# Kernel optimization log

Measured on AMD Instinct MI355X. Metric: run time of the kernel, lower is better.

Reference implementation:

```python
import jax, jax.numpy as jnp
import numpy as np
import math

N_HEADS = 8
LN_EPS = 1e-5

def _layernorm(x, g, b):
    m = jnp.mean(x, axis=-1, keepdims=True)
    v = jnp.var(x, axis=-1, keepdims=True)
    return (x - m) / jnp.sqrt(v + LN_EPS) * g + b

def _elu_feature(x):
    return jax.nn.elu(x) + 1.0

def _recurrence(Q, K, V, decay, reverse):
    # Q,K,V: (B,H,T,d); decay: (H,)
    B, H, T, d = Q.shape
    lamS = decay[None, :, None, None]
    lamz = decay[None, :, None]
    def step(carry, inp):
        S, z = carry
        q, k, v = inp
        S = lamS * S + k[..., :, None] * v[..., None, :]       # (B,H,d,d)
        z = lamz * z + k                                        # (B,H,d)
        y_raw = jnp.einsum('bhd,bhde->bhe', q, S)
        c_raw = jnp.sum(q * z, axis=-1)
        qk = jnp.sum(q * k, axis=-1, keepdims=True)
        return (S, z), (y_raw - 0.5 * qk * v, c_raw - 0.5 * qk[..., 0])
    S0 = jnp.zeros((B, H, d, d), Q.dtype)
    z0 = jnp.zeros((B, H, d), Q.dtype)
    qs = jnp.moveaxis(Q, 2, 0)
    ks = jnp.moveaxis(K, 2, 0)
    vs = jnp.moveaxis(V, 2, 0)
    _, (Y, C) = jax.lax.scan(step, (S0, z0), (qs, ks, vs), reverse=reverse)
    return jnp.moveaxis(Y, 0, 2), jnp.moveaxis(C, 0, 2)  # (B,H,T,d),(B,H,T)

def setup_inputs() -> dict:
    B, T, D, F = 2, 2048, 512, 2048
    key = jax.random.key(0)
    ks = jax.random.split(key, 8)
    std = 0.02
    return {
        'x': jax.random.normal(ks[0], (B, T, D), jnp.float32),
        'mask': jnp.zeros((B, T), dtype=bool),
        'Wq': jax.random.normal(ks[1], (D, D), jnp.float32) * std,
        'Wk': jax.random.normal(ks[2], (D, D), jnp.float32) * std,
        'Wv': jax.random.normal(ks[3], (D, D), jnp.float32) * std,
        'Wo': jax.random.normal(ks[4], (D, D), jnp.float32) * std,
        'bo': jnp.zeros((D,), jnp.float32),
        'g1': jnp.ones((D,), jnp.float32),
        'b1': jnp.zeros((D,), jnp.float32),
        'g2': jnp.ones((D,), jnp.float32),
        'b2': jnp.zeros((D,), jnp.float32),
        'W1': jax.random.normal(ks[5], (F, D), jnp.float32) * std,
        'bf1': jnp.zeros((F,), jnp.float32),
        'W2': jax.random.normal(ks[6], (D, F), jnp.float32) * std,
        'bf2': jnp.zeros((D,), jnp.float32),
        'decay_logit': jnp.full((N_HEADS,), math.log(9.0), jnp.float32),
    }

def reference(x, mask, Wq, Wk, Wv, Wo, bo, g1, b1, g2, b2, W1, bf1, W2, bf2, decay_logit):
    B, T, D = x.shape
    H = N_HEADS
    hd = D // H
    residual = x
    xn = _layernorm(x, g1, b1)
    def proj(W):
        return jnp.einsum('btd,od->bto', xn, W).reshape(B, T, H, hd).transpose(0, 2, 1, 3)
    Q = _elu_feature(proj(Wq))
    K = _elu_feature(proj(Wk))
    V = proj(Wv)
    pad = (~mask).astype(x.dtype)[:, None, :, None]  # (B,1,T,1)
    K = K * pad
    V = V * pad
    decay = jax.nn.sigmoid(decay_logit)
    Yf, Cf = _recurrence(Q, K, V, decay, reverse=False)
    Yb, Cb = _recurrence(Q, K, V, decay, reverse=True)
    denom = jnp.clip((Cf + Cb)[..., None], 1e-6)
    out = (Yf + Yb) / denom                       # (B,H,T,d)
    out = out.transpose(0, 2, 1, 3).reshape(B, T, D)
    out = jnp.einsum('btd,od->bto', out, Wo) + bo
    x = residual + out
    h = _layernorm(x, g2, b2)
    ffn = jnp.einsum('btd,fd->btf', h, W1) + bf1
    ffn = jax.nn.gelu(ffn, approximate=False)
    ffn = jnp.einsum('btf,df->btd', ffn, W2) + bf2
    return x + ffn
```

## Files before the change

kernel.cpp:

```cpp
#include <hip/hip_runtime.h>
#include <math.h>

#define BB 2
#define TT 2048
#define DD 512
#define FF 2048
#define HH 8
#define BT 4096
#define NC 32
#define CK 64

typedef __bf16 bf16_t;
typedef bf16_t bf16x8 __attribute__((ext_vector_type(8)));
typedef bf16_t bf16x4 __attribute__((ext_vector_type(4)));
typedef float f32x4 __attribute__((ext_vector_type(4)));

typedef const __attribute__((address_space(1))) void* gas_p;
typedef __attribute__((address_space(3))) void* las_p;

__device__ __forceinline__ void async16(const void* g, void* l) {
  __builtin_amdgcn_global_load_lds((gas_p)g, (las_p)l, 16, 0, 0);
}

#define PIPE_SYNC(vm) asm volatile("s_waitcnt lgkmcnt(0) vmcnt(" vm ")\n\ts_barrier" ::: "memory")

__global__ __launch_bounds__(256) void ln_cast_kernel(
    const float* __restrict__ x, const float* __restrict__ g, const float* __restrict__ bb,
    bf16_t* __restrict__ out,
    const float* __restrict__ Wq, const float* __restrict__ Wk,
    const float* __restrict__ Wv, const float* __restrict__ Wo,
    const float* __restrict__ W1, const float* __restrict__ W2,
    bf16_t* __restrict__ wdst) {
  int t = threadIdx.x;
  if (blockIdx.x >= 1024) {
    size_t i = ((size_t)(blockIdx.x - 1024) * 256 + t) * 8;
    const float* src; size_t off;
    if (i < 262144)       { src = Wq; off = i; }
    else if (i < 524288)  { src = Wk; off = i - 262144; }
    else if (i < 786432)  { src = Wv; off = i - 524288; }
    else if (i < 1048576) { src = Wo; off = i - 786432; }
    else if (i < 2097152) { src = W1; off = i - 1048576; }
    else                  { src = W2; off = i - 2097152; }
    float4 a = *(const float4*)(src + off);
    float4 b = *(const float4*)(src + off + 4);
    bf16x8 o;
    o[0] = (bf16_t)a.x; o[1] = (bf16_t)a.y; o[2] = (bf16_t)a.z; o[3] = (bf16_t)a.w;
    o[4] = (bf16_t)b.x; o[5] = (bf16_t)b.y; o[6] = (bf16_t)b.z; o[7] = (bf16_t)b.w;
    *(bf16x8*)(wdst + i) = o;
    return;
  }
  int w = t >> 6, l = t & 63;
  int row = blockIdx.x * 4 + w;
  int c0 = l * 8;
  const float* xr = x + (size_t)row * DD + c0;
  float4 a = *(const float4*)xr;
  float4 b4 = *(const float4*)(xr + 4);
  float s  = a.x + a.y + a.z + a.w + b4.x + b4.y + b4.z + b4.w;
  float sq = a.x*a.x + a.y*a.y + a.z*a.z + a.w*a.w +
             b4.x*b4.x + b4.y*b4.y + b4.z*b4.z + b4.w*b4.w;
  for (int o = 32; o; o >>= 1) { s += __shfl_xor(s, o); sq += __shfl_xor(sq, o); }
  float m = s * (1.f / 512.f);
  float var = sq * (1.f / 512.f) - m * m;
  float r = rsqrtf(var + 1e-5f);
  float4 ga = *(const float4*)(g + c0);  float4 gb = *(const float4*)(g + c0 + 4);
  float4 ba = *(const float4*)(bb + c0); float4 bbv = *(const float4*)(bb + c0 + 4);
  bf16x8 o8;
  o8[0] = (bf16_t)((a.x - m) * r * ga.x + ba.x);
  o8[1] = (bf16_t)((a.y - m) * r * ga.y + ba.y);
  o8[2] = (bf16_t)((a.z - m) * r * ga.z + ba.z);
  o8[3] = (bf16_t)((a.w - m) * r * ga.w + ba.w);
  o8[4] = (bf16_t)((b4.x - m) * r * gb.x + bbv.x);
  o8[5] = (bf16_t)((b4.y - m) * r * gb.y + bbv.y);
  o8[6] = (bf16_t)((b4.z - m) * r * gb.z + bbv.z);
  o8[7] = (bf16_t)((b4.w - m) * r * gb.w + bbv.w);
  *(bf16x8*)(out + (size_t)row * DD + c0) = o8;
}

__global__ __launch_bounds__(256) void ln2_kernel(
    const float* __restrict__ x2, const float* __restrict__ g, const float* __restrict__ bb,
    bf16_t* __restrict__ out) {
  int t = threadIdx.x;
  int w = t >> 6, l = t & 63;
  int row = blockIdx.x * 4 + w;
  int c0 = l * 8;
  const float* xr = x2 + (size_t)row * DD + c0;
  float4 a = *(const float4*)xr;
  float4 b4 = *(const float4*)(xr + 4);
  float s  = a.x + a.y + a.z + a.w + b4.x + b4.y + b4.z + b4.w;
  float sq = a.x*a.x + a.y*a.y + a.z*a.z + a.w*a.w +
             b4.x*b4.x + b4.y*b4.y + b4.z*b4.z + b4.w*b4.w;
  for (int o = 32; o; o >>= 1) { s += __shfl_xor(s, o); sq += __shfl_xor(sq, o); }
  float m = s * (1.f / 512.f);
  float var = sq * (1.f / 512.f) - m * m;
  float r = rsqrtf(var + 1e-5f);
  float4 ga = *(const float4*)(g + c0);  float4 gb = *(const float4*)(g + c0 + 4);
  float4 ba = *(const float4*)(bb + c0); float4 bbv = *(const float4*)(bb + c0 + 4);
  bf16x8 o8;
  o8[0] = (bf16_t)((a.x - m) * r * ga.x + ba.x);
  o8[1] = (bf16_t)((a.y - m) * r * ga.y + ba.y);
  o8[2] = (bf16_t)((a.z - m) * r * ga.z + ba.z);
  o8[3] = (bf16_t)((a.w - m) * r * ga.w + ba.w);
  o8[4] = (bf16_t)((b4.x - m) * r * gb.x + bbv.x);
  o8[5] = (bf16_t)((b4.y - m) * r * gb.y + bbv.y);
  o8[6] = (bf16_t)((b4.z - m) * r * gb.z + bbv.z);
  o8[7] = (bf16_t)((b4.w - m) * r * gb.w + bbv.w);
  *(bf16x8*)(out + (size_t)row * DD + c0) = o8;
}

template<int MODE>
__global__ __launch_bounds__(256) void mfma_gemm(
    const bf16_t* __restrict__ A, const bf16_t* __restrict__ B, int K, int NT,
    bf16_t* __restrict__ Qo, bf16_t* __restrict__ Ko, bf16_t* __restrict__ Vo,
    bf16_t* __restrict__ Ob, const float* __restrict__ bias,
    const unsigned char* __restrict__ mask) {
  __shared__ __align__(16) bf16_t smem[3 * 8192];
  int tid = threadIdx.x;
  int bid = blockIdx.x;
  int xcd = bid & 7;
  int tmp = bid >> 3;
  int nt = tmp % NT;
  int mt = (tmp / NT) * 8 + xcd;
  int n0 = nt * 128, m0 = mt * 128;
  int elt = tid * 8;
  int srow = elt >> 5, scol = elt & 31;
  const bf16_t* Ag = A + (size_t)(m0 + srow) * K + scol;
  const bf16_t* Bg = B + (size_t)(n0 + srow) * K + scol;
  size_t hstep = (size_t)64 * K;
  int NS = K >> 5;
#define ISSUE(s) { bf16_t* st = smem + ((s) % 3) * 8192; int k0 = (s) * 32; \
    async16(Ag + k0, st + elt); async16(Ag + k0 + hstep, st + 2048 + elt); \
    async16(Bg + k0, st + 4096 + elt); async16(Bg + k0 + hstep, st + 6144 + elt); }
  ISSUE(0); ISSUE(1);
  f32x4 acc[4][4] = {};
  int w = tid >> 6, l = tid & 63;
  int wm = (w >> 1) * 64, wn = (w & 1) * 64;
  int fr = l & 15, fk = (l >> 4) * 8;
  for (int i = 0; i < NS; i++) {
    if (i < NS - 1) PIPE_SYNC("4");
    else            PIPE_SYNC("0");
    if (i + 2 < NS) ISSUE(i + 2);
    const bf16_t* As = smem + (i % 3) * 8192;
    const bf16_t* Bs = As + 4096;
    bf16x8 af[4], bfr[4];
#pragma unroll
    for (int ii = 0; ii < 4; ii++) af[ii] = *(const bf16x8*)&As[(wm + ii * 16 + fr) * 32 + fk];
#pragma unroll
    for (int j = 0; j < 4; j++) bfr[j] = *(const bf16x8*)&Bs[(wn + j * 16 + fr) * 32 + fk];
#pragma unroll
    for (int ii = 0; ii < 4; ii++)
#pragma unroll
      for (int j = 0; j < 4; j++)
        acc[ii][j] = __builtin_amdgcn_mfma_f32_16x16x32_bf16(af[ii], bfr[j], acc[ii][j], 0, 0, 0);
  }
#undef ISSUE
  __syncthreads();
  const int CST = 136;
  int cn = l & 15, cr = (l >> 4) * 4;
  bf16_t* outp;
  int ldc, ncol0;
  if (MODE == 0) {
    int seg = n0 >> 9;
    outp = seg == 0 ? Qo : (seg == 1 ? Ko : Vo);
    ldc = 512; ncol0 = n0 & 511;
  } else {
    outp = Ob; ldc = 2048; ncol0 = n0;
  }
#pragma unroll
  for (int i = 0; i < 4; i++) {
#pragma unroll
    for (int r = 0; r < 4; r++) {
      int mrow = wm + i * 16 + cr + r;
      float p = 1.f;
      if (MODE == 0) p = mask[m0 + mrow] ? 0.f : 1.f;
#pragma unroll
      for (int j = 0; j < 4; j++) {
        int ncol = wn + j * 16 + cn;
        float v = acc[i][j][r];
        float ov;
        if (MODE == 0) {
          int seg = n0 >> 9;
          float e = v > 0.f ? v + 1.f : expf(v);
          ov = seg == 0 ? e : (seg == 1 ? e * p : v * p);
        } else {
          float t2 = v + bias[ncol0 + ncol];
          ov = 0.5f * t2 * (1.f + erff(t2 * 0.70710678118654752f));
        }
        smem[mrow * CST + ncol] = (bf16_t)ov;
      }
    }
  }
  __syncthreads();
#pragma unroll
  for (int it = 0; it < 8; it++) {
    int vec = tid + it * 256;
    int row = vec >> 4;
    int col = (vec & 15) * 8;
    bf16x8 v8 = *(const bf16x8*)&smem[row * CST + col];
    *(bf16x8*)(outp + (size_t)(m0 + row) * ldc + ncol0 + col) = v8;
  }
}

template<int MODE>
__global__ __launch_bounds__(256) void gemm64(
    const bf16_t* __restrict__ A, const bf16_t* __restrict__ B, int K, int NT,
    bf16_t* __restrict__ Qo, bf16_t* __restrict__ Ko, bf16_t* __restrict__ Vo,
    const float* __restrict__ bias, const float* __restrict__ resid,
    float* __restrict__ fout, const unsigned char* __restrict__ mask) {
  __shared__ __align__(16) bf16_t smem[4 * 6144];
  int tid = threadIdx.x;
  int bid = blockIdx.x;
  int xcd = bid & 7;
  int tmp = bid >> 3;
  int nt = tmp % NT;
  int mt = (tmp / NT) * 8 + xcd;
  int n0 = nt * 64, m0 = mt * 128;
  int elt = tid * 8;
  int srow = elt >> 5, scol = elt & 31;
  const bf16_t* Ag = A + (size_t)(m0 + srow) * K + scol;
  const bf16_t* Bg = B + (size_t)(n0 + srow) * K + scol;
  size_t hstep = (size_t)64 * K;
  const int NS = K >> 5;
#define ISSUE(s) { bf16_t* st = smem + ((s) & 3) * 6144; int k0 = (s) * 32; \
    async16(Ag + k0, st + elt); async16(Ag + k0 + hstep, st + 2048 + elt); \
    async16(Bg + k0, st + 4096 + elt); }
  ISSUE(0); ISSUE(1); ISSUE(2);
  f32x4 acc[4][2] = {};
  int w = tid >> 6, l = tid & 63;
  int wm = (w >> 1) * 64, wn = (w & 1) * 32;
  int fr = l & 15, fk = (l >> 4) * 8;
  for (int i = 0; i < NS; i++) {
    int rem = NS - 1 - i;
    if (rem >= 2)      PIPE_SYNC("6");
    else if (rem == 1) PIPE_SYNC("3");
    else               PIPE_SYNC("0");
    if (i + 3 < NS) ISSUE(i + 3);
    const bf16_t* As = smem + (i & 3) * 6144;
    const bf16_t* Bs = As + 4096;
    bf16x8 af[4], bfr[2];
#pragma unroll
    for (int ii = 0; ii < 4; ii++) af[ii] = *(const bf16x8*)&As[(wm + ii * 16 + fr) * 32 + fk];
#pragma unroll
    for (int j = 0; j < 2; j++) bfr[j] = *(const bf16x8*)&Bs[(wn + j * 16 + fr) * 32 + fk];
#pragma unroll
    for (int ii = 0; ii < 4; ii++)
#pragma unroll
      for (int j = 0; j < 2; j++)
        acc[ii][j] = __builtin_amdgcn_mfma_f32_16x16x32_bf16(af[ii], bfr[j], acc[ii][j], 0, 0, 0);
  }
#undef ISSUE
  __syncthreads();
  int cn = l & 15, cr = (l >> 4) * 4;
  if (MODE == 0) {
    const int CST = 72;
    int seg = n0 >> 9;
#pragma unroll
    for (int i = 0; i < 4; i++) {
#pragma unroll
      for (int r = 0; r < 4; r++) {
        int mrow = wm + i * 16 + cr + r;
        float p = mask[m0 + mrow] ? 0.f : 1.f;
#pragma unroll
        for (int j = 0; j < 2; j++) {
          int ncol = wn + j * 16 + cn;
          float v = acc[i][j][r];
          float e = v > 0.f ? v + 1.f : expf(v);
          float ov = seg == 0 ? e : (seg == 1 ? e * p : v * p);
          smem[mrow * CST + ncol] = (bf16_t)ov;
        }
      }
    }
    __syncthreads();
    bf16_t* outp = seg == 0 ? Qo : (seg == 1 ? Ko : Vo);
    int ncol0 = n0 & 511;
#pragma unroll
    for (int it = 0; it < 4; it++) {
      int vec = tid + it * 256;
      int row = vec >> 3;
      int col = (vec & 7) * 8;
      bf16x8 v8 = *(const bf16x8*)&smem[row * CST + col];
      *(bf16x8*)(outp + (size_t)(m0 + row) * 512 + ncol0 + col) = v8;
    }
  } else {
    const int FST = 72;
    float* smf = (float*)smem;
#pragma unroll
    for (int i = 0; i < 4; i++)
#pragma unroll
      for (int r = 0; r < 4; r++) {
        int mrow = wm + i * 16 + cr + r;
#pragma unroll
        for (int j = 0; j < 2; j++) {
          int ncol = wn + j * 16 + cn;
          smf[mrow * FST + ncol] = acc[i][j][r];
        }
      }
    __syncthreads();
#pragma unroll
    for (int it = 0; it < 8; it++) {
      int vec = tid + it * 256;
      int row = vec >> 4;
      int col = (vec & 15) * 4;
      size_t gidx = (size_t)(m0 + row) * 512 + n0 + col;
      float4 v = *(const float4*)&smf[row * FST + col];
      float4 bi = *(const float4*)(bias + n0 + col);
      float4 rr = *(const float4*)(resid + gidx);
      *(float4*)(fout + gidx) = make_float4(v.x + bi.x + rr.x, v.y + bi.y + rr.y,
                                            v.z + bi.z + rr.z, v.w + bi.w + rr.w);
    }
  }
}

__global__ __launch_bounds__(256) void chunk_summary_kernel(
    const bf16_t* __restrict__ Kb, const bf16_t* __restrict__ Vb,
    const float* __restrict__ dl, bf16_t* __restrict__ Sst, float* __restrict__ zst) {
  int chunk = blockIdx.x, bh = blockIdx.y;
  int b = bh >> 3, h = bh & 7;
  int t0 = chunk * CK;
  int tid = threadIdx.x;
  const int ST = 72;
  __shared__ __align__(16) bf16_t KTf[64 * ST];
  __shared__ __align__(16) bf16_t KTb[64 * ST];
  __shared__ __align__(16) bf16_t VT [64 * ST];
  float lam = 1.f / (1.f + expf(-dl[h]));
  int lrow = tid >> 2, lq = tid & 3;
  float wf = powf(lam, (float)(63 - lrow));
  float wb = powf(lam, (float)lrow);
#pragma unroll
  for (int q = 0; q < 2; q++) {
    int c = lq * 16 + q * 8;
    size_t gidx = ((size_t)(b * TT + t0 + lrow)) * DD + (size_t)h * 64 + c;
    bf16x8 k8 = *(const bf16x8*)(Kb + gidx);
    bf16x8 v8 = *(const bf16x8*)(Vb + gidx);
#pragma unroll
    for (int u = 0; u < 8; u++) {
      float kv = (float)k8[u];
      KTf[(c + u) * ST + lrow] = (bf16_t)(kv * wf);
      KTb[(c + u) * ST + lrow] = (bf16_t)(kv * wb);
      VT [(c + u) * ST + lrow] = v8[u];
    }
  }
  __syncthreads();
  int w = tid >> 6, l = tid & 63;
  int dir = w >> 1;
  int drow = (w & 1) * 32;
  const bf16_t* KT = dir ? KTb : KTf;
  int fr = l & 15, fk = (l >> 4) * 8;
  bf16x8 afrag[2][2], bfrag[4][2];
#pragma unroll
  for (int ti = 0; ti < 2; ti++) {
    afrag[ti][0] = *(const bf16x8*)&KT[(drow + ti * 16 + fr) * ST + fk];
    afrag[ti][1] = *(const bf16x8*)&KT[(drow + ti * 16 + fr) * ST + 32 + fk];
  }
#pragma unroll
  for (int tj = 0; tj < 4; tj++) {
    bfrag[tj][0] = *(const bf16x8*)&VT[(tj * 16 + fr) * ST + fk];
    bfrag[tj][1] = *(const bf16x8*)&VT[(tj * 16 + fr) * ST + 32 + fk];
  }
  f32x4 acc[2][4] = {};
#pragma unroll
  for (int ti = 0; ti < 2; ti++)
#pragma unroll
    for (int tj = 0; tj < 4; tj++) {
      acc[ti][tj] = __builtin_amdgcn_mfma_f32_16x16x32_bf16(afrag[ti][0], bfrag[tj][0], acc[ti][tj], 0, 0, 0);
      acc[ti][tj] = __builtin_amdgcn_mfma_f32_16x16x32_bf16(afrag[ti][1], bfrag[tj][1], acc[ti][tj], 0, 0, 0);
    }
  if (tid < 128) {
    const bf16_t* KTz = (tid >> 6) ? KTb : KTf;
    int d = tid & 63;
    float z = 0.f;
    for (int j = 0; j < 64; j += 8) {
      bf16x8 kz = *(const bf16x8*)&KTz[d * ST + j];
#pragma unroll
      for (int u = 0; u < 8; u++) z += (float)kz[u];
    }
    zst[(((size_t)(tid >> 6) * 16 + bh) * NC + chunk) * 64 + d] = z;
  }
  __syncthreads();
  bf16_t* Ss = dir ? KTb : KTf;
  int cr = (l >> 4) * 4, cn = l & 15;
#pragma unroll
  for (int ti = 0; ti < 2; ti++)
#pragma unroll
    for (int tj = 0; tj < 4; tj++)
#pragma unroll
      for (int r = 0; r < 4; r++) {
        int d = drow + ti * 16 + cr + r;
        int e = tj * 16 + cn;
        Ss[e * ST + d] = (bf16_t)acc[ti][tj][r];
      }
  __syncthreads();
  size_t bfr = ((size_t)bh * NC + chunk) * 4096;
  size_t bbr = (((size_t)16 + bh) * NC + chunk) * 4096;
#pragma unroll
  for (int it = 0; it < 4; it++) {
    int vec = tid + it * 256;
    int d2 = vec >> 9;
    int idx = vec & 511;
    int row = idx >> 3, col = (idx & 7) * 8;
    bf16x8 v8 = *(const bf16x8*)((d2 ? KTb : KTf) + row * ST + col);
    *(bf16x8*)(Sst + (d2 ? bbr : bfr) + (size_t)row * 64 + col) = v8;
  }
}

__global__ __launch_bounds__(256) void scan_kernel(bf16_t* __restrict__ Sst,
                                                   float* __restrict__ zst,
                                                   const float* __restrict__ dl) {
  int sub = blockIdx.x;
  int bh  = blockIdx.y;
  int dir = blockIdx.z;
  int h = bh & 7;
  int tid = threadIdx.x;
  float lam = 1.f / (1.f + expf(-dl[h]));
  float lamC = powf(lam, 64.f);
  int elem = sub * 256 + tid;
  size_t base = ((size_t)dir * 16 + bh) * (size_t)NC * 4096 + elem;
  float s = 0.f;
  for (int g = 0; g < 4; g++) {
    bf16_t L[8];
#pragma unroll
    for (int i = 0; i < 8; i++) {
      int st = g * 8 + i;
      int c = dir ? (NC - 1 - st) : st;
      L[i] = Sst[base + (size_t)c * 4096];
    }
#pragma unroll
    for (int i = 0; i < 8; i++) {
      int st = g * 8 + i;
      int c = dir ? (NC - 1 - st) : st;
      s = s * lamC + (float)L[i];
      Sst[base + (size_t)c * 4096] = (bf16_t)s;
    }
  }
  if (sub == 0 && tid < 64) {
    size_t zb = ((size_t)dir * 16 + bh) * (size_t)NC * 64 + tid;
    float z = 0.f;
    for (int g = 0; g < 4; g++) {
      float zL[8];
#pragma unroll
      for (int i = 0; i < 8; i++) {
        int st = g * 8 + i;
        int c = dir ? (NC - 1 - st) : st;
        zL[i] = zst[zb + (size_t)c * 64];
      }
#pragma unroll
      for (int i = 0; i < 8; i++) {
        int st = g * 8 + i;
        int c = dir ? (NC - 1 - st) : st;
        z = z * lamC + zL[i];
        zst[zb + (size_t)c * 64] = z;
      }
    }
  }
}

#define AST 72
__global__ __launch_bounds__(256) void chunk_attn_kernel(
    const bf16_t* __restrict__ Qb, const bf16_t* __restrict__ Kb, const bf16_t* __restrict__ Vb,
    const bf16_t* __restrict__ Sst, const float* __restrict__ zst, const float* __restrict__ dl,
    bf16_t* __restrict__ attnb) {
  int chunk = blockIdx.x, bh = blockIdx.y;
  int b = bh >> 3, h = bh & 7;
  int t0 = chunk * CK;
  int tid = threadIdx.x;
  __shared__ __align__(16) bf16_t Qa[64 * AST];
  __shared__ __align__(16) bf16_t KA[64 * AST];
  __shared__ __align__(16) bf16_t Vt[64 * AST];
  __shared__ __align__(16) bf16_t Sft[64 * AST];
  __shared__ __align__(16) bf16_t Sbt[64 * AST];
  __shared__ float rowpart[64][16];
  __shared__ float zpf[64], zpb[64];
  __shared__ float den[64];
  __shared__ float pw[72];
  float lam = 1.f / (1.f + expf(-dl[h]));
  if (tid <= 64) pw[tid] = powf(lam, (float)tid);
  int lrow = tid >> 2, lq = tid & 3;
  for (int q = 0; q < 2; q++) {
    int c = lq * 16 + q * 8;
    size_t g = ((size_t)(b * TT + t0 + lrow)) * DD + (size_t)h * 64 + c;
    bf16x8 q8 = *(const bf16x8*)(Qb + g);
    bf16x8 k8 = *(const bf16x8*)(Kb + g);
    bf16x8 v8 = *(const bf16x8*)(Vb + g);
    *(bf16x8*)&Qa[lrow * AST + c] = q8;
    *(bf16x8*)&KA[lrow * AST + c] = k8;
#pragma unroll
    for (int u = 0; u < 8; u++) Vt[(c + u) * AST + lrow] = v8[u];
  }
  {
    int c16 = lq * 16;
    if (chunk > 0) {
      const bf16_t* src = Sst + ((size_t)bh * NC + chunk - 1) * 4096 + (size_t)lrow * 64 + c16;
      *(bf16x8*)&Sft[lrow * AST + c16] = *(const bf16x8*)src;
      *(bf16x8*)&Sft[lrow * AST + c16 + 8] = *(const bf16x8*)(src + 8);
      if (tid < 64) zpf[tid] = zst[((size_t)bh * NC + chunk - 1) * 64 + tid];
    } else {
      bf16x8 z8 = {};
      *(bf16x8*)&Sft[lrow * AST + c16] = z8;
      *(bf16x8*)&Sft[lrow * AST + c16 + 8] = z8;
      if (tid < 64) zpf[tid] = 0.f;
    }
    if (chunk < NC - 1) {
      const bf16_t* src = Sst + (((size_t)16 + bh) * NC + chunk + 1) * 4096 + (size_t)lrow * 64 + c16;
      *(bf16x8*)&Sbt[lrow * AST + c16] = *(const bf16x8*)src;
      *(bf16x8*)&Sbt[lrow * AST + c16 + 8] = *(const bf16x8*)(src + 8);
      if (tid < 64) zpb[tid] = zst[(((size_t)16 + bh) * NC + chunk + 1) * 64 + tid];
    } else {
      bf16x8 z8 = {};
      *(bf16x8*)&Sbt[lrow * AST + c16] = z8;
      *(bf16x8*)&Sbt[lrow * AST + c16 + 8] = z8;
      if (tid < 64) zpb[tid] = 0.f;
    }
  }
  __syncthreads();
  int w = tid >> 6, l = tid & 63;
  int fr = l & 15, fk = (l >> 4) * 8;
  int cr = (l >> 4) * 4, cn = l & 15;
  int ms = w * 16;
  bf16x8 qf0 = *(const bf16x8*)&Qa[(ms + fr) * AST + fk];
  bf16x8 qf1 = *(const bf16x8*)&Qa[(ms + fr) * AST + 32 + fk];
  f32x4 aqk[4] = {};
#pragma unroll
  for (int t = 0; t < 4; t++) {
    bf16x8 kf0 = *(const bf16x8*)&KA[(t * 16 + fr) * AST + fk];
    bf16x8 kf1 = *(const bf16x8*)&KA[(t * 16 + fr) * AST + 32 + fk];
    aqk[t] = __builtin_amdgcn_mfma_f32_16x16x32_bf16(qf0, kf0, aqk[t], 0, 0, 0);
    aqk[t] = __builtin_amdgcn_mfma_f32_16x16x32_bf16(qf1, kf1, aqk[t], 0, 0, 0);
  }
  __syncthreads();
  float rs[4] = {0.f, 0.f, 0.f, 0.f};
#pragma unroll
  for (int t = 0; t < 4; t++) {
#pragma unroll
    for (int r = 0; r < 4; r++) {
      int i = ms + cr + r;
      int j = t * 16 + cn;
      int dd = i > j ? i - j : j - i;
      float v = aqk[t][r] * pw[dd];
      rs[r] += v;
      KA[i * AST + j] = (bf16_t)v;
    }
  }
#pragma unroll
  for (int r = 0; r < 4; r++) rowpart[ms + cr + r][cn] = rs[r];
  __syncthreads();
  bf16x8 af0 = *(const bf16x8*)&KA[(ms + fr) * AST + fk];
  bf16x8 af1 = *(const bf16x8*)&KA[(ms + fr) * AST + 32 + fk];
  f32x4 aY[4] = {}, aSf[4] = {}, aSb[4] = {};
#pragma unroll
  for (int t = 0; t < 4; t++) {
    bf16x8 vf0 = *(const bf16x8*)&Vt[(t * 16 + fr) * AST + fk];
    bf16x8 vf1 = *(const bf16x8*)&Vt[(t * 16 + fr) * AST + 32 + fk];
    aY[t] = __builtin_amdgcn_mfma_f32_16x16x32_bf16(af0, vf0, aY[t], 0, 0, 0);
    aY[t] = __builtin_amdgcn_mfma_f32_16x16x32_bf16(af1, vf1, aY[t], 0, 0, 0);
    bf16x8 sf0 = *(const bf16x8*)&Sft[(t * 16 + fr) * AST + fk];
    bf16x8 sf1 = *(const bf16x8*)&Sft[(t * 16 + fr) * AST + 32 + fk];
    aSf[t] = __builtin_amdgcn_mfma_f32_16x16x32_bf16(qf0, sf0, aSf[t], 0, 0, 0);
    aSf[t] = __builtin_amdgcn_mfma_f32_16x16x32_bf16(qf1, sf1, aSf[t], 0, 0, 0);
    bf16x8 sb0 = *(const bf16x8*)&Sbt[(t * 16 + fr) * AST + fk];
    bf16x8 sb1 = *(const bf16x8*)&Sbt[(t * 16 + fr) * AST + 32 + fk];
    aSb[t] = __builtin_amdgcn_mfma_f32_16x16x32_bf16(qf0, sb0, aSb[t], 0, 0, 0);
    aSb[t] = __builtin_amdgcn_mfma_f32_16x16x32_bf16(qf1, sb1, aSb[t], 0, 0, 0);
  }
  {
    int i = tid >> 2, p = tid & 3;
    float s = 0.f;
#pragma unroll
    for (int xx = 0; xx < 4; xx++) s += rowpart[i][p * 4 + xx];
    float czf = 0.f, czb = 0.f;
#pragma unroll
    for (int cc = 0; cc < 2; cc++) {
      int c = p * 16 + cc * 8;
      bf16x8 q8 = *(const bf16x8*)&Qa[i * AST + c];
#pragma unroll
      for (int u = 0; u < 8; u++) { czf += (float)q8[u] * zpf[c + u]; czb += (float)q8[u] * zpb[c + u]; }
    }
    float dsum = s + pw[i + 1] * czf + pw[64 - i] * czb;
    dsum += __shfl_xor(dsum, 1);
    dsum += __shfl_xor(dsum, 2);
    if (p == 0) den[i] = dsum;
  }
  __syncthreads();
#pragma unroll
  for (int t = 0; t < 4; t++) {
#pragma unroll
    for (int r = 0; r < 4; r++) {
      int i = ms + cr + r;
      int e = t * 16 + cn;
      float lrf = pw[i + 1], lrb = pw[64 - i];
      float inv = 1.f / fmaxf(den[i], 1e-6f);
      float val = (aY[t][r] + lrf * aSf[t][r] + lrb * aSb[t][r]) * inv;
      attnb[((size_t)(b * TT + t0 + i)) * DD + (size_t)h * 64 + e] = (bf16_t)val;
    }
  }
}

extern "C" void kernel_launch(void* const* d_in, const int* in_sizes, int n_in,
                              void* d_out, int out_size, void* d_ws, size_t ws_size,
                              hipStream_t stream) {
  const float* x   = (const float*)d_in[0];
  const unsigned char* mask = (const unsigned char*)d_in[1];
  const float* Wq  = (const float*)d_in[2];
  const float* Wk  = (const float*)d_in[3];
  const float* Wv  = (const float*)d_in[4];
  const float* Wo  = (const float*)d_in[5];
  const float* bo  = (const float*)d_in[6];
  const float* g1  = (const float*)d_in[7];
  const float* b1  = (const float*)d_in[8];
  const float* g2  = (const float*)d_in[9];
  const float* b2  = (const float*)d_in[10];
  const float* W1  = (const float*)d_in[11];
  const float* bf1 = (const float*)d_in[12];
  const float* W2  = (const float*)d_in[13];
  const float* bf2 = (const float*)d_in[14];
  const float* dl  = (const float*)d_in[15];
  float* out = (float*)d_out;

  float* ws = (float*)d_ws;
  const size_t U = (size_t)BT * DD;
  float* Qr  = ws;
  float* Kr  = ws + U;
  float* Vr  = ws + 2 * U;
  float* R3  = ws + 3 * U;
  float* R4  = ws + 4 * U;
  float* x2  = ws + 5 * U;
  bf16_t* Sstb = (bf16_t*)(ws + 6 * U);
  float* zst = ws + 8 * U;
  bf16_t* wall = (bf16_t*)(ws + 8 * U + 131072);
  bf16_t* Qb    = (bf16_t*)Qr;
  bf16_t* Kb    = (bf16_t*)Kr;
  bf16_t* Vb    = (bf16_t*)Vr;
  bf16_t* xnb   = (bf16_t*)R3;
  bf16_t* attnb = (bf16_t*)R4;
  bf16_t* h2b   = (bf16_t*)Qr;
  bf16_t* ffn1b = (bf16_t*)Kr;
  bf16_t* Wob = wall + 786432;
  bf16_t* W1b = wall + 1048576;
  bf16_t* W2b = wall + 2097152;

  ln_cast_kernel<<<1024 + 1536, 256, 0, stream>>>(x, g1, b1, xnb, Wq, Wk, Wv, Wo, W1, W2, wall);
  gemm64<0><<<768, 256, 0, stream>>>(xnb, wall, 512, 24, Qb, Kb, Vb,
                                     nullptr, nullptr, nullptr, mask);
  chunk_summary_kernel<<<dim3(NC, 16), 256, 0, stream>>>(Kb, Vb, dl, Sstb, zst);
  scan_kernel<<<dim3(16, 16, 2), 256, 0, stream>>>(Sstb, zst, dl);
  chunk_attn_kernel<<<dim3(NC, 16), 256, 0, stream>>>(Qb, Kb, Vb, Sstb, zst, dl, attnb);
  gemm64<1><<<256, 256, 0, stream>>>(attnb, Wob, 512, 8, nullptr, nullptr, nullptr,
                                     bo, x, x2, nullptr);
  ln2_kernel<<<1024, 256, 0, stream>>>(x2, g2, b2, h2b);
  mfma_gemm<2><<<512, 256, 0, stream>>>(h2b, W1b, 512, 16, nullptr, nullptr, nullptr,
                                        ffn1b, bf1, nullptr);
  gemm64<1><<<256, 256, 0, stream>>>(ffn1b, W2b, 2048, 8, nullptr, nullptr, nullptr,
                                     bf2, x2, out, nullptr);
}
```

Measured before the change: 184.3 us.

## Fuse chunk summary, scan and chunk attention into one cooperative kernel

Merges the three attention-stage kernels into one cooperative kernel of 512 blocks, using grid-wide syncs between the chunk-summary, inter-chunk scan and intra-chunk attention phases. Q, K and V are loaded into shared memory once and reused, instead of being reloaded by separate launches. This removes two kernel launch boundaries and the associated reloads, at the cost of grid-sync overhead, higher shared-memory use per block, and a requirement that all 512 blocks be co-resident.

```diff
diff --git a/kernel.cpp b/kernel.cpp
--- a/kernel.cpp
+++ b/kernel.cpp
@@ -1,4 +1,5 @@
 #include <hip/hip_runtime.h>
+#include <hip/hip_cooperative_groups.h>
 #include <math.h>
 
 #define BB 2
@@ -310,18 +311,27 @@
   }
 }
 
-__global__ __launch_bounds__(256) void chunk_summary_kernel(
-    const bf16_t* __restrict__ Kb, const bf16_t* __restrict__ Vb,
-    const float* __restrict__ dl, bf16_t* __restrict__ Sst, float* __restrict__ zst) {
-  int chunk = blockIdx.x, bh = blockIdx.y;
+#define MST 72
+__global__ __launch_bounds__(256, 2) void attn_mega_kernel(
+    const bf16_t* __restrict__ Qb, const bf16_t* __restrict__ Kb, const bf16_t* __restrict__ Vb,
+    const float* __restrict__ dl, bf16_t* __restrict__ Sst, float* __restrict__ zst,
+    bf16_t* __restrict__ attnb) {
+  __shared__ __align__(16) bf16_t KT2[2][64 * MST];
+  __shared__ __align__(16) bf16_t VT [64 * MST];
+  __shared__ __align__(16) bf16_t KA [64 * MST];
+  __shared__ __align__(16) bf16_t Qa [64 * MST];
+  __shared__ __align__(16) bf16_t Sft[64 * MST];
+  __shared__ __align__(16) bf16_t Sbt[64 * MST];
+  __shared__ float rowpart[64][16];
+  __shared__ float zpf[64], zpb[64], den[64];
+  __shared__ float pw[72];
+  int tid = threadIdx.x;
+  int bid = blockIdx.x;
+  int chunk = bid & 31, bh = bid >> 5;
   int b = bh >> 3, h = bh & 7;
   int t0 = chunk * CK;
-  int tid = threadIdx.x;
-  const int ST = 72;
-  __shared__ __align__(16) bf16_t KTf[64 * ST];
-  __shared__ __align__(16) bf16_t KTb[64 * ST];
-  __shared__ __align__(16) bf16_t VT [64 * ST];
   float lam = 1.f / (1.f + expf(-dl[h]));
+  if (tid <= 64) pw[tid] = powf(lam, (float)tid);
   int lrow = tid >> 2, lq = tid & 3;
   float wf = powf(lam, (float)(63 - lrow));
   float wb = powf(lam, (float)lrow);
@@ -329,199 +339,165 @@
   for (int q = 0; q < 2; q++) {
     int c = lq * 16 + q * 8;
     size_t gidx = ((size_t)(b * TT + t0 + lrow)) * DD + (size_t)h * 64 + c;
+    bf16x8 q8 = *(const bf16x8*)(Qb + gidx);
     bf16x8 k8 = *(const bf16x8*)(Kb + gidx);
     bf16x8 v8 = *(const bf16x8*)(Vb + gidx);
+    *(bf16x8*)&Qa[lrow * MST + c] = q8;
+    *(bf16x8*)&KA[lrow * MST + c] = k8;
 #pragma unroll
     for (int u = 0; u < 8; u++) {
       float kv = (float)k8[u];
-      KTf[(c + u) * ST + lrow] = (bf16_t)(kv * wf);
-      KTb[(c + u) * ST + lrow] = (bf16_t)(kv * wb);
-      VT [(c + u) * ST + lrow] = v8[u];
+      KT2[0][(c + u) * MST + lrow] = (bf16_t)(kv * wf);
+      KT2[1][(c + u) * MST + lrow] = (bf16_t)(kv * wb);
+      VT [(c + u) * MST + lrow] = v8[u];
     }
   }
   __syncthreads();
   int w = tid >> 6, l = tid & 63;
   int dir = w >> 1;
   int drow = (w & 1) * 32;
-  const bf16_t* KT = dir ? KTb : KTf;
   int fr = l & 15, fk = (l >> 4) * 8;
-  bf16x8 afrag[2][2], bfrag[4][2];
-#pragma unroll
-  for (int ti = 0; ti < 2; ti++) {
-    afrag[ti][0] = *(const bf16x8*)&KT[(drow + ti * 16 + fr) * ST + fk];
-    afrag[ti][1] = *(const bf16x8*)&KT[(drow + ti * 16 + fr) * ST + 32 + fk];
-  }
-#pragma unroll
-  for (int tj = 0; tj < 4; tj++) {
-    bfrag[tj][0] = *(const bf16x8*)&VT[(tj * 16 + fr) * ST + fk];
-    bfrag[tj][1] = *(const bf16x8*)&VT[(tj * 16 + fr) * ST + 32 + fk];
-  }
-  f32x4 acc[2][4] = {};
-#pragma unroll
-  for (int ti = 0; ti < 2; ti++)
+  int cr = (l >> 4) * 4, cn = l & 15;
+  {
+    const bf16_t* KT = KT2[dir];
+    bf16x8 afrag[2][2], bfrag[4][2];
+#pragma unroll
+    for (int ti = 0; ti < 2; ti++) {
+      afrag[ti][0] = *(const bf16x8*)&KT[(drow + ti * 16 + fr) * MST + fk];
+      afrag[ti][1] = *(const bf16x8*)&KT[(drow + ti * 16 + fr) * MST + 32 + fk];
+    }
 #pragma unroll
     for (int tj = 0; tj < 4; tj++) {
-      acc[ti][tj] = __builtin_amdgcn_mfma_f32_16x16x32_bf16(afrag[ti][0], bfrag[tj][0], acc[ti][tj], 0, 0, 0);
-      acc[ti][tj] = __builtin_amdgcn_mfma_f32_16x16x32_bf16(afrag[ti][1], bfrag[tj][1], acc[ti][tj], 0, 0, 0);
-    }
-  if (tid < 128) {
-    const bf16_t* KTz = (tid >> 6) ? KTb : KTf;
-    int d = tid & 63;
-    float z = 0.f;
-    for (int j = 0; j < 64; j += 8) {
-      bf16x8 kz = *(const bf16x8*)&KTz[d * ST + j];
-#pragma unroll
-      for (int u = 0; u < 8; u++) z += (float)kz[u];
-    }
-    zst[(((size_t)(tid >> 6) * 16 + bh) * NC + chunk) * 64 + d] = z;
-  }
-  __syncthreads();
-  bf16_t* Ss = dir ? KTb : KTf;
-  int cr = (l >> 4) * 4, cn = l & 15;
-#pragma unroll
-  for (int ti = 0; ti < 2; ti++)
-#pragma unroll
-    for (int tj = 0; tj < 4; tj++)
-#pragma unroll
-      for (int r = 0; r < 4; r++) {
-        int d = drow + ti * 16 + cr + r;
-        int e = tj * 16 + cn;
-        Ss[e * ST + d] = (bf16_t)acc[ti][tj][r];
-      }
-  __syncthreads();
-  size_t bfr = ((size_t)bh * NC + chunk) * 4096;
-  size_t bbr = (((size_t)16 + bh) * NC + chunk) * 4096;
-#pragma unroll
-  for (int it = 0; it < 4; it++) {
-    int vec = tid + it * 256;
-    int d2 = vec >> 9;
-    int idx = vec & 511;
-    int row = idx >> 3, col = (idx & 7) * 8;
-    bf16x8 v8 = *(const bf16x8*)((d2 ? KTb : KTf) + row * ST + col);
-    *(bf16x8*)(Sst + (d2 ? bbr : bfr) + (size_t)row * 64 + col) = v8;
-  }
-}
-
-__global__ __launch_bounds__(256) void scan_kernel(bf16_t* __restrict__ Sst,
-                                                   float* __restrict__ zst,
-                                                   const float* __restrict__ dl) {
-  int sub = blockIdx.x;
-  int bh  = blockIdx.y;
-  int dir = blockIdx.z;
-  int h = bh & 7;
-  int tid = threadIdx.x;
-  float lam = 1.f / (1.f + expf(-dl[h]));
-  float lamC = powf(lam, 64.f);
-  int elem = sub * 256 + tid;
-  size_t base = ((size_t)dir * 16 + bh) * (size_t)NC * 4096 + elem;
-  float s = 0.f;
-  for (int g = 0; g < 4; g++) {
-    bf16_t L[8];
-#pragma unroll
-    for (int i = 0; i < 8; i++) {
-      int st = g * 8 + i;
-      int c = dir ? (NC - 1 - st) : st;
-      L[i] = Sst[base + (size_t)c * 4096];
-    }
-#pragma unroll
-    for (int i = 0; i < 8; i++) {
-      int st = g * 8 + i;
-      int c = dir ? (NC - 1 - st) : st;
-      s = s * lamC + (float)L[i];
-      Sst[base + (size_t)c * 4096] = (bf16_t)s;
-    }
-  }
-  if (sub == 0 && tid < 64) {
-    size_t zb = ((size_t)dir * 16 + bh) * (size_t)NC * 64 + tid;
-    float z = 0.f;
+      bfrag[tj][0] = *(const bf16x8*)&VT[(tj * 16 + fr) * MST + fk];
+      bfrag[tj][1] = *(const bf16x8*)&VT[(tj * 16 + fr) * MST + 32 + fk];
+    }
+    f32x4 acc[2][4] = {};
+#pragma unroll
+    for (int ti = 0; ti < 2; ti++)
+#pragma unroll
+      for (int tj = 0; tj < 4; tj++) {
+        acc[ti][tj] = __builtin_amdgcn_mfma_f32_16x16x32_bf16(afrag[ti][0], bfrag[tj][0], acc[ti][tj], 0, 0, 0);
+        acc[ti][tj] = __builtin_amdgcn_mfma_f32_16x16x32_bf16(afrag[ti][1], bfrag[tj][1], acc[ti][tj], 0, 0, 0);
+      }
+    if (tid < 128) {
+      const bf16_t* KTz = KT2[tid >> 6];
+      int d = tid & 63;
+      float z = 0.f;
+      for (int j = 0; j < 64; j += 8) {
+        bf16x8 kz = *(const bf16x8*)&KTz[d * MST + j];
+#pragma unroll
+        for (int u = 0; u < 8; u++) z += (float)kz[u];
+      }
+      zst[(((size_t)(tid >> 6) * 16 + bh) * NC + chunk) * 64 + d] = z;
+    }
+    __syncthreads();
+    bf16_t* Ss = KT2[dir];
+#pragma unroll
+    for (int ti = 0; ti < 2; ti++)
+#pragma unroll
+      for (int tj = 0; tj < 4; tj++)
+#pragma unroll
+        for (int r = 0; r < 4; r++) {
+          int d = drow + ti * 16 + cr + r;
+          int e = tj * 16 + cn;
+          Ss[e * MST + d] = (bf16_t)acc[ti][tj][r];
+        }
+    __syncthreads();
+    size_t bfrow = ((size_t)bh * NC + chunk) * 4096;
+    size_t bbrow = (((size_t)16 + bh) * NC + chunk) * 4096;
+#pragma unroll
+    for (int it = 0; it < 4; it++) {
+      int vec = tid + it * 256;
+      int d2 = vec >> 9;
+      int idx = vec & 511;
+      int row = idx >> 3, col = (idx & 7) * 8;
+      bf16x8 v8 = *(const bf16x8*)&KT2[d2][row * MST + col];
+      *(bf16x8*)(Sst + (d2 ? bbrow : bfrow) + (size_t)row * 64 + col) = v8;
+    }
+  }
+  cooperative_groups::this_grid().sync();
+  {
+    int sub2 = bid & 15;
+    int bh2  = (bid >> 4) & 15;
+    int dir2 = bid >> 8;
+    int h2 = bh2 & 7;
+    float lam2 = 1.f / (1.f + expf(-dl[h2]));
+    float lamC = powf(lam2, 64.f);
+    int elem = sub2 * 256 + tid;
+    size_t base = ((size_t)dir2 * 16 + bh2) * (size_t)NC * 4096 + elem;
+    float s = 0.f;
     for (int g = 0; g < 4; g++) {
-      float zL[8];
+      bf16_t L[8];
 #pragma unroll
       for (int i = 0; i < 8; i++) {
         int st = g * 8 + i;
-        int c = dir ? (NC - 1 - st) : st;
-        zL[i] = zst[zb + (size_t)c * 64];
+        int c = dir2 ? (NC - 1 - st) : st;
+        L[i] = Sst[base + (size_t)c * 4096];
       }
 #pragma unroll
       for (int i = 0; i < 8; i++) {
         int st = g * 8 + i;
-        int c = dir ? (NC - 1 - st) : st;
-        z = z * lamC + zL[i];
-        zst[zb + (size_t)c * 64] = z;
-      }
-    }
-  }
-}
-
-#define AST 72
-__global__ __launch_bounds__(256) void chunk_attn_kernel(
-    const bf16_t* __restrict__ Qb, const bf16_t* __restrict__ Kb, const bf16_t* __restrict__ Vb,
-    const bf16_t* __restrict__ Sst, const float* __restrict__ zst, const float* __restrict__ dl,
-    bf16_t* __restrict__ attnb) {
-  int chunk = blockIdx.x, bh = blockIdx.y;
-  int b = bh >> 3, h = bh & 7;
-  int t0 = chunk * CK;
-  int tid = threadIdx.x;
-  __shared__ __align__(16) bf16_t Qa[64 * AST];
-  __shared__ __align__(16) bf16_t KA[64 * AST];
-  __shared__ __align__(16) bf16_t Vt[64 * AST];
-  __shared__ __align__(16) bf16_t Sft[64 * AST];
-  __shared__ __align__(16) bf16_t Sbt[64 * AST];
-  __shared__ float rowpart[64][16];
-  __shared__ float zpf[64], zpb[64];
-  __shared__ float den[64];
-  __shared__ float pw[72];
-  float lam = 1.f / (1.f + expf(-dl[h]));
-  if (tid <= 64) pw[tid] = powf(lam, (float)tid);
-  int lrow = tid >> 2, lq = tid & 3;
-  for (int q = 0; q < 2; q++) {
-    int c = lq * 16 + q * 8;
-    size_t g = ((size_t)(b * TT + t0 + lrow)) * DD + (size_t)h * 64 + c;
-    bf16x8 q8 = *(const bf16x8*)(Qb + g);
-    bf16x8 k8 = *(const bf16x8*)(Kb + g);
-    bf16x8 v8 = *(const bf16x8*)(Vb + g);
-    *(bf16x8*)&Qa[lrow * AST + c] = q8;
-    *(bf16x8*)&KA[lrow * AST + c] = k8;
-#pragma unroll
-    for (int u = 0; u < 8; u++) Vt[(c + u) * AST + lrow] = v8[u];
-  }
+        int c = dir2 ? (NC - 1 - st) : st;
+        s = s * lamC + (float)L[i];
+        Sst[base + (size_t)c * 4096] = (bf16_t)s;
+      }
+    }
+    if (sub2 == 0 && tid < 64) {
+      size_t zb = ((size_t)dir2 * 16 + bh2) * (size_t)NC * 64 + tid;
+      float z = 0.f;
+      for (int g = 0; g < 4; g++) {
+        float zL[8];
+#pragma unroll
+        for (int i = 0; i < 8; i++) {
+          int st = g * 8 + i;
+          int c = dir2 ? (NC - 1 - st) : st;
+          zL[i] = zst[zb + (size_t)c * 64];
+        }
+#pragma unroll
+        for (int i = 0; i < 8; i++) {
+          int st = g * 8 + i;
+          int c = dir2 ? (NC - 1 - st) : st;
+          z = z * lamC + zL[i];
+          zst[zb + (size_t)c * 64] = z;
+        }
+      }
+    }
+  }
+  cooperative_groups::this_grid().sync();
   {
     int c16 = lq * 16;
     if (chunk > 0) {
       const bf16_t* src = Sst + ((size_t)bh * NC + chunk - 1) * 4096 + (size_t)lrow * 64 + c16;
-      *(bf16x8*)&Sft[lrow * AST + c16] = *(const bf16x8*)src;
-      *(bf16x8*)&Sft[lrow * AST + c16 + 8] = *(const bf16x8*)(src + 8);
+      *(bf16x8*)&Sft[lrow * MST + c16] = *(const bf16x8*)src;
+      *(bf16x8*)&Sft[lrow * MST + c16 + 8] = *(const bf16x8*)(src + 8);
       if (tid < 64) zpf[tid] = zst[((size_t)bh * NC + chunk - 1) * 64 + tid];
     } else {
       bf16x8 z8 = {};
-      *(bf16x8*)&Sft[lrow * AST + c16] = z8;
-      *(bf16x8*)&Sft[lrow * AST + c16 + 8] = z8;
+      *(bf16x8*)&Sft[lrow * MST + c16] = z8;
+      *(bf16x8*)&Sft[lrow * MST + c16 + 8] = z8;
       if (tid < 64) zpf[tid] = 0.f;
     }
     if (chunk < NC - 1) {
       const bf16_t* src = Sst + (((size_t)16 + bh) * NC + chunk + 1) * 4096 + (size_t)lrow * 64 + c16;
-      *(bf16x8*)&Sbt[lrow * AST + c16] = *(const bf16x8*)src;
-      *(bf16x8*)&Sbt[lrow * AST + c16 + 8] = *(const bf16x8*)(src + 8);
+      *(bf16x8*)&Sbt[lrow * MST + c16] = *(const bf16x8*)src;
+      *(bf16x8*)&Sbt[lrow * MST + c16 + 8] = *(const bf16x8*)(src + 8);
       if (tid < 64) zpb[tid] = zst[(((size_t)16 + bh) * NC + chunk + 1) * 64 + tid];
     } else {
       bf16x8 z8 = {};
-      *(bf16x8*)&Sbt[lrow * AST + c16] = z8;
-      *(bf16x8*)&Sbt[lrow * AST + c16 + 8] = z8;
+      *(bf16x8*)&Sbt[lrow * MST + c16] = z8;
+      *(bf16x8*)&Sbt[lrow * MST + c16 + 8] = z8;
       if (tid < 64) zpb[tid] = 0.f;
     }
   }
   __syncthreads();
-  int w = tid >> 6, l = tid & 63;
-  int fr = l & 15, fk = (l >> 4) * 8;
-  int cr = (l >> 4) * 4, cn = l & 15;
   int ms = w * 16;
-  bf16x8 qf0 = *(const bf16x8*)&Qa[(ms + fr) * AST + fk];
-  bf16x8 qf1 = *(const bf16x8*)&Qa[(ms + fr) * AST + 32 + fk];
+  bf16x8 qf0 = *(const bf16x8*)&Qa[(ms + fr) * MST + fk];
+  bf16x8 qf1 = *(const bf16x8*)&Qa[(ms + fr) * MST + 32 + fk];
   f32x4 aqk[4] = {};
 #pragma unroll
   for (int t = 0; t < 4; t++) {
-    bf16x8 kf0 = *(const bf16x8*)&KA[(t * 16 + fr) * AST + fk];
-    bf16x8 kf1 = *(const bf16x8*)&KA[(t * 16 + fr) * AST + 32 + fk];
+    bf16x8 kf0 = *(const bf16x8*)&KA[(t * 16 + fr) * MST + fk];
+    bf16x8 kf1 = *(const bf16x8*)&KA[(t * 16 + fr) * MST + 32 + fk];
     aqk[t] = __builtin_amdgcn_mfma_f32_16x16x32_bf16(qf0, kf0, aqk[t], 0, 0, 0);
     aqk[t] = __builtin_amdgcn_mfma_f32_16x16x32_bf16(qf1, kf1, aqk[t], 0, 0, 0);
   }
@@ -536,27 +512,27 @@
       int dd = i > j ? i - j : j - i;
       float v = aqk[t][r] * pw[dd];
       rs[r] += v;
-      KA[i * AST + j] = (bf16_t)v;
+      KA[i * MST + j] = (bf16_t)v;
     }
   }
 #pragma unroll
   for (int r = 0; r < 4; r++) rowpart[ms + cr + r][cn] = rs[r];
   __syncthreads();
-  bf16x8 af0 = *(const bf16x8*)&KA[(ms + fr) * AST + fk];
-  bf16x8 af1 = *(const bf16x8*)&KA[(ms + fr) * AST + 32 + fk];
+  bf16x8 af0 = *(const bf16x8*)&KA[(ms + fr) * MST + fk];
+  bf16x8 af1 = *(const bf16x8*)&KA[(ms + fr) * MST + 32 + fk];
   f32x4 aY[4] = {}, aSf[4] = {}, aSb[4] = {};
 #pragma unroll
   for (int t = 0; t < 4; t++) {
-    bf16x8 vf0 = *(const bf16x8*)&Vt[(t * 16 + fr) * AST + fk];
-    bf16x8 vf1 = *(const bf16x8*)&Vt[(t * 16 + fr) * AST + 32 + fk];
+    bf16x8 vf0 = *(const bf16x8*)&VT[(t * 16 + fr) * MST + fk];
+    bf16x8 vf1 = *(const bf16x8*)&VT[(t * 16 + fr) * MST + 32 + fk];
     aY[t] = __builtin_amdgcn_mfma_f32_16x16x32_bf16(af0, vf0, aY[t], 0, 0, 0);
     aY[t] = __builtin_amdgcn_mfma_f32_16x16x32_bf16(af1, vf1, aY[t], 0, 0, 0);
-    bf16x8 sf0 = *(const bf16x8*)&Sft[(t * 16 + fr) * AST + fk];
-    bf16x8 sf1 = *(const bf16x8*)&Sft[(t * 16 + fr) * AST + 32 + fk];
+    bf16x8 sf0 = *(const bf16x8*)&Sft[(t * 16 + fr) * MST + fk];
+    bf16x8 sf1 = *(const bf16x8*)&Sft[(t * 16 + fr) * MST + 32 + fk];
     aSf[t] = __builtin_amdgcn_mfma_f32_16x16x32_bf16(qf0, sf0, aSf[t], 0, 0, 0);
     aSf[t] = __builtin_amdgcn_mfma_f32_16x16x32_bf16(qf1, sf1, aSf[t], 0, 0, 0);
-    bf16x8 sb0 = *(const bf16x8*)&Sbt[(t * 16 + fr) * AST + fk];
-    bf16x8 sb1 = *(const bf16x8*)&Sbt[(t * 16 + fr) * AST + 32 + fk];
+    bf16x8 sb0 = *(const bf16x8*)&Sbt[(t * 16 + fr) * MST + fk];
+    bf16x8 sb1 = *(const bf16x8*)&Sbt[(t * 16 + fr) * MST + 32 + fk];
     aSb[t] = __builtin_amdgcn_mfma_f32_16x16x32_bf16(qf0, sb0, aSb[t], 0, 0, 0);
     aSb[t] = __builtin_amdgcn_mfma_f32_16x16x32_bf16(qf1, sb1, aSb[t], 0, 0, 0);
   }
@@ -569,7 +545,7 @@
 #pragma unroll
     for (int cc = 0; cc < 2; cc++) {
       int c = p * 16 + cc * 8;
-      bf16x8 q8 = *(const bf16x8*)&Qa[i * AST + c];
+      bf16x8 q8 = *(const bf16x8*)&Qa[i * MST + c];
 #pragma unroll
       for (int u = 0; u < 8; u++) { czf += (float)q8[u] * zpf[c + u]; czb += (float)q8[u] * zpb[c + u]; }
     }
@@ -639,9 +615,12 @@
   ln_cast_kernel<<<1024 + 1536, 256, 0, stream>>>(x, g1, b1, xnb, Wq, Wk, Wv, Wo, W1, W2, wall);
   gemm64<0><<<768, 256, 0, stream>>>(xnb, wall, 512, 24, Qb, Kb, Vb,
                                      nullptr, nullptr, nullptr, mask);
-  chunk_summary_kernel<<<dim3(NC, 16), 256, 0, stream>>>(Kb, Vb, dl, Sstb, zst);
-  scan_kernel<<<dim3(16, 16, 2), 256, 0, stream>>>(Sstb, zst, dl);
-  chunk_attn_kernel<<<dim3(NC, 16), 256, 0, stream>>>(Qb, Kb, Vb, Sstb, zst, dl, attnb);
+  {
+    const bf16_t* Qb_ = Qb; const bf16_t* Kb_ = Kb; const bf16_t* Vb_ = Vb;
+    const float* dl_ = dl; bf16_t* Sst_ = Sstb; float* zst_ = zst; bf16_t* attnb_ = attnb;
+    void* margs[] = { &Qb_, &Kb_, &Vb_, &dl_, &Sst_, &zst_, &attnb_ };
+    hipLaunchCooperativeKernel((void*)attn_mega_kernel, dim3(512), dim3(256), margs, 0, stream);
+  }
   gemm64<1><<<256, 256, 0, stream>>>(attnb, Wob, 512, 8, nullptr, nullptr, nullptr,
                                      bo, x, x2, nullptr);
   ln2_kernel<<<1024, 256, 0, stream>>>(x2, g2, b2, h2b);
```

After: 345.5 us. +87.5%, slower.

## Fold inter-chunk state scan into chunk attention kernel via direct weighted sums

Applied to the files above, without the earlier changes.

Removes the separate scan kernel that built prefix states across chunks. Each chunk_attn block now computes its forward and backward incoming state directly, as a decay-weighted sum of all earlier (or later) chunk summaries read from global memory, with the z vectors handled the same way. This saves a kernel launch and the read-modify-write pass over the state buffer. The cost is O(NC^2) total reads instead of O(NC), plus load imbalance, since blocks near the ends loop over up to 31 chunks.

```diff
diff --git a/kernel.cpp b/kernel.cpp
--- a/kernel.cpp
+++ b/kernel.cpp
@@ -402,57 +402,6 @@
   }
 }
 
-__global__ __launch_bounds__(256) void scan_kernel(bf16_t* __restrict__ Sst,
-                                                   float* __restrict__ zst,
-                                                   const float* __restrict__ dl) {
-  int sub = blockIdx.x;
-  int bh  = blockIdx.y;
-  int dir = blockIdx.z;
-  int h = bh & 7;
-  int tid = threadIdx.x;
-  float lam = 1.f / (1.f + expf(-dl[h]));
-  float lamC = powf(lam, 64.f);
-  int elem = sub * 256 + tid;
-  size_t base = ((size_t)dir * 16 + bh) * (size_t)NC * 4096 + elem;
-  float s = 0.f;
-  for (int g = 0; g < 4; g++) {
-    bf16_t L[8];
-#pragma unroll
-    for (int i = 0; i < 8; i++) {
-      int st = g * 8 + i;
-      int c = dir ? (NC - 1 - st) : st;
-      L[i] = Sst[base + (size_t)c * 4096];
-    }
-#pragma unroll
-    for (int i = 0; i < 8; i++) {
-      int st = g * 8 + i;
-      int c = dir ? (NC - 1 - st) : st;
-      s = s * lamC + (float)L[i];
-      Sst[base + (size_t)c * 4096] = (bf16_t)s;
-    }
-  }
-  if (sub == 0 && tid < 64) {
-    size_t zb = ((size_t)dir * 16 + bh) * (size_t)NC * 64 + tid;
-    float z = 0.f;
-    for (int g = 0; g < 4; g++) {
-      float zL[8];
-#pragma unroll
-      for (int i = 0; i < 8; i++) {
-        int st = g * 8 + i;
-        int c = dir ? (NC - 1 - st) : st;
-        zL[i] = zst[zb + (size_t)c * 64];
-      }
-#pragma unroll
-      for (int i = 0; i < 8; i++) {
-        int st = g * 8 + i;
-        int c = dir ? (NC - 1 - st) : st;
-        z = z * lamC + zL[i];
-        zst[zb + (size_t)c * 64] = z;
-      }
-    }
-  }
-}
-
 #define AST 72
 __global__ __launch_bounds__(256) void chunk_attn_kernel(
     const bf16_t* __restrict__ Qb, const bf16_t* __restrict__ Kb, const bf16_t* __restrict__ Vb,
@@ -487,27 +436,50 @@
   }
   {
     int c16 = lq * 16;
-    if (chunk > 0) {
-      const bf16_t* src = Sst + ((size_t)bh * NC + chunk - 1) * 4096 + (size_t)lrow * 64 + c16;
-      *(bf16x8*)&Sft[lrow * AST + c16] = *(const bf16x8*)src;
-      *(bf16x8*)&Sft[lrow * AST + c16 + 8] = *(const bf16x8*)(src + 8);
-      if (tid < 64) zpf[tid] = zst[((size_t)bh * NC + chunk - 1) * 64 + tid];
-    } else {
-      bf16x8 z8 = {};
-      *(bf16x8*)&Sft[lrow * AST + c16] = z8;
-      *(bf16x8*)&Sft[lrow * AST + c16 + 8] = z8;
-      if (tid < 64) zpf[tid] = 0.f;
-    }
-    if (chunk < NC - 1) {
-      const bf16_t* src = Sst + (((size_t)16 + bh) * NC + chunk + 1) * 4096 + (size_t)lrow * 64 + c16;
-      *(bf16x8*)&Sbt[lrow * AST + c16] = *(const bf16x8*)src;
-      *(bf16x8*)&Sbt[lrow * AST + c16 + 8] = *(const bf16x8*)(src + 8);
-      if (tid < 64) zpb[tid] = zst[(((size_t)16 + bh) * NC + chunk + 1) * 64 + tid];
-    } else {
-      bf16x8 z8 = {};
-      *(bf16x8*)&Sbt[lrow * AST + c16] = z8;
-      *(bf16x8*)&Sbt[lrow * AST + c16 + 8] = z8;
-      if (tid < 64) zpb[tid] = 0.f;
+    float lamC = powf(lam, 64.f);
+    float accf[16], accb[16];
+#pragma unroll
+    for (int u = 0; u < 16; u++) { accf[u] = 0.f; accb[u] = 0.f; }
+    size_t off = (size_t)lrow * 64 + c16;
+    const bf16_t* basef = Sst + (size_t)bh * NC * 4096 + off;
+    const bf16_t* baseb = Sst + ((size_t)16 + bh) * NC * 4096 + off;
+    float wgt = 1.f;
+    for (int j = chunk - 1; j >= 0; j--) {
+      bf16x8 a0 = *(const bf16x8*)(basef + (size_t)j * 4096);
+      bf16x8 a1 = *(const bf16x8*)(basef + (size_t)j * 4096 + 8);
+#pragma unroll
+      for (int u = 0; u < 8; u++) { accf[u] += wgt * (float)a0[u]; accf[8 + u] += wgt * (float)a1[u]; }
+      wgt *= lamC;
+    }
+    wgt = 1.f;
+    for (int j = chunk + 1; j < NC; j++) {
+      bf16x8 a0 = *(const bf16x8*)(baseb + (size_t)j * 4096);
+      bf16x8 a1 = *(const bf16x8*)(baseb + (size_t)j * 4096 + 8);
+#pragma unroll
+      for (int u = 0; u < 8; u++) { accb[u] += wgt * (float)a0[u]; accb[8 + u] += wgt * (float)a1[u]; }
+      wgt *= lamC;
+    }
+    bf16x8 f0, f1, b0, b1;
+#pragma unroll
+    for (int u = 0; u < 8; u++) {
+      f0[u] = (bf16_t)accf[u]; f1[u] = (bf16_t)accf[8 + u];
+      b0[u] = (bf16_t)accb[u]; b1[u] = (bf16_t)accb[8 + u];
+    }
+    *(bf16x8*)&Sft[lrow * AST + c16] = f0;
+    *(bf16x8*)&Sft[lrow * AST + c16 + 8] = f1;
+    *(bf16x8*)&Sbt[lrow * AST + c16] = b0;
+    *(bf16x8*)&Sbt[lrow * AST + c16 + 8] = b1;
+    if (tid < 128) {
+      int d2 = tid >> 6, d = tid & 63;
+      size_t zb = ((size_t)d2 * 16 + bh) * (size_t)NC * 64 + d;
+      float z = 0.f, wz = 1.f;
+      if (d2 == 0) {
+        for (int j = chunk - 1; j >= 0; j--) { z += wz * zst[zb + (size_t)j * 64]; wz *= lamC; }
+        zpf[d] = z;
+      } else {
+        for (int j = chunk + 1; j < NC; j++) { z += wz * zst[zb + (size_t)j * 64]; wz *= lamC; }
+        zpb[d] = z;
+      }
     }
   }
   __syncthreads();
@@ -640,7 +612,6 @@
   gemm64<0><<<768, 256, 0, stream>>>(xnb, wall, 512, 24, Qb, Kb, Vb,
                                      nullptr, nullptr, nullptr, mask);
   chunk_summary_kernel<<<dim3(NC, 16), 256, 0, stream>>>(Kb, Vb, dl, Sstb, zst);
-  scan_kernel<<<dim3(16, 16, 2), 256, 0, stream>>>(Sstb, zst, dl);
   chunk_attn_kernel<<<dim3(NC, 16), 256, 0, stream>>>(Qb, Kb, Vb, Sstb, zst, dl, attnb);
   gemm64<1><<<256, 256, 0, stream>>>(attnb, Wob, 512, 8, nullptr, nullptr, nullptr,
                                      bo, x, x2, nullptr);
```

After: 194.2 us. 5.4% more time.
